# Kernel tuning notes

Hardware: AMD Instinct MI355X
Metric: run time of the kernel (lower is better)

## Reference

```python
import jax, jax.numpy as jnp
import numpy as np

H = 50  # hidden_size
IN = 3  # input_size
OUT = 7


def _lstm_layer(x, Wih, Whh, bih, bhh):
    # x: [B, T, D]; Wih: [4H, D]; Whh: [4H, H]; biases: [4H]
    # Precompute input-side gate pre-activations once (torch adds both biases).
    xg = jnp.einsum('btd,gd->btg', x, Wih) + bih + bhh  # [B, T, 4H]
    B = x.shape[0]
    h0 = jnp.zeros((B, H), x.dtype)
    c0 = jnp.zeros((B, H), x.dtype)

    def step(carry, xt):
        h, c = carry
        gates = xt + h @ Whh.T  # [B, 4H]
        i, f, g, o = jnp.split(gates, 4, axis=-1)  # torch gate order: i,f,g,o
        i = jax.nn.sigmoid(i)
        f = jax.nn.sigmoid(f)
        g = jnp.tanh(g)
        o = jax.nn.sigmoid(o)
        c = f * c + i * g
        h = o * jnp.tanh(c)
        return (h, c), h

    (_, _), hs = jax.lax.scan(step, (h0, c0), jnp.swapaxes(xg, 0, 1))  # hs: [T, B, H]
    return jnp.swapaxes(hs, 0, 1)  # [B, T, H]


def setup_inputs() -> dict:
    key = jax.random.key(0)
    ks = jax.random.split(key, 11)
    s = 1.0 / np.sqrt(H)  # torch LSTM init scale
    B, T = 4096, 512
    return {
        'x': jax.random.normal(ks[0], (B, T, IN), jnp.float32),
        'Wih0': jax.random.uniform(ks[1], (4 * H, IN), jnp.float32, -s, s),
        'Whh0': jax.random.uniform(ks[2], (4 * H, H), jnp.float32, -s, s),
        'bih0': jax.random.uniform(ks[3], (4 * H,), jnp.float32, -s, s),
        'bhh0': jax.random.uniform(ks[4], (4 * H,), jnp.float32, -s, s),
        'Wih1': jax.random.uniform(ks[5], (4 * H, H), jnp.float32, -s, s),
        'Whh1': jax.random.uniform(ks[6], (4 * H, H), jnp.float32, -s, s),
        'bih1': jax.random.uniform(ks[7], (4 * H,), jnp.float32, -s, s),
        'bhh1': jax.random.uniform(ks[8], (4 * H,), jnp.float32, -s, s),
        'Wfc': jax.random.uniform(ks[9], (OUT, H), jnp.float32, -s, s),
        'bfc': jax.random.uniform(ks[10], (OUT,), jnp.float32, -s, s),
    }


def reference(x, Wih0, Whh0, bih0, bhh0, Wih1, Whh1, bih1, bhh1, Wfc, bfc):
    h1 = _lstm_layer(x, Wih0, Whh0, bih0, bhh0)   # [B, T, H]
    h2 = _lstm_layer(h1, Wih1, Whh1, bih1, bhh1)  # [B, T, H]
    last = h2[:, -1, :]                           # [B, H]
    return last @ Wfc.T + bfc                     # [B, 7]
```

## Files before the change

kernel.cpp:

```cpp
#include <hip/hip_runtime.h>

#define HD 50
#define TT 512
#define BRR 16
#define TC 32
#define HS 72

using f16   = _Float16;
using f16x8 = __attribute__((ext_vector_type(8))) f16;
using f32x4 = __attribute__((ext_vector_type(4))) float;

__device__ __forceinline__ short f2h_bits(float f) {
    f16 h = (f16)f;
    return *reinterpret_cast<short*>(&h);
}
__device__ __forceinline__ float h2f(short b) {
    f16 h = *reinterpret_cast<f16*>(&b);
    return (float)h;
}
__device__ __forceinline__ float frcp(float x) { return __builtin_amdgcn_rcpf(x); }
__device__ __forceinline__ float sigf(float x) { return frcp(1.0f + __expf(-x)); }
__device__ __forceinline__ float tanhfast(float x) {
    return 1.0f - 2.0f * frcp(__expf(2.0f * x) + 1.0f);
}

__global__ __launch_bounds__(512, 2) void lstm2_f16(
    const float* __restrict__ x,
    const float* __restrict__ Wih0, const float* __restrict__ Whh0,
    const float* __restrict__ bih0, const float* __restrict__ bhh0,
    const float* __restrict__ Wih1, const float* __restrict__ Whh1,
    const float* __restrict__ bih1, const float* __restrict__ bhh1,
    const float* __restrict__ Wfc, const float* __restrict__ bfc,
    float* __restrict__ out)
{
    __shared__ short s_h0[2][BRR][HS];
    __shared__ short s_h1[2][BRR][HS];
    __shared__ float s_xs[2][BRR][TC*3];

    const int tid  = threadIdx.x;
    const int wid  = tid >> 6;
    const int lane = tid & 63;
    const int lr   = lane & 15;
    const int lq   = lane >> 4;
    const int r0   = blockIdx.x * BRR;
    const bool pathA = (wid < 4);
    const int  wsub  = wid & 3;
    const int  u     = lr * 4 + wsub;
    const bool valid = (u < HD);

    f16x8 bw[4][4];
    float bvT[4];
    #pragma unroll
    for (int tt = 0; tt < 4; ++tt) {
        #pragma unroll
        for (int s = 0; s < 4; ++s) bw[tt][s] = (f16x8)0;
        const int g = tt * HD + (valid ? u : 0);
        if (pathA) {
            bvT[tt] = valid ? bih0[g] + bhh0[g] : 0.f;
            #pragma unroll
            for (int s = 0; s < 2; ++s) {
                #pragma unroll
                for (int j = 0; j < 8; ++j) {
                    const int k = s*32 + lq*8 + j;
                    float wv = 0.f;
                    if (valid) {
                        if (k < HD) wv = Whh0[g*HD + k];
                        else if (k < HD+3) wv = Wih0[g*3 + (k-HD)];
                    }
                    bw[tt][s][j] = (f16)wv;
                }
            }
        } else {
            bvT[tt] = valid ? bih1[g] + bhh1[g] : 0.f;
            #pragma unroll
            for (int s = 0; s < 4; ++s) {
                #pragma unroll
                for (int j = 0; j < 8; ++j) {
                    const int k = s*32 + lq*8 + j;
                    float wv = 0.f;
                    if (valid) {
                        if (k < HD) wv = Wih1[g*HD + k];
                        else if (k >= 64 && k < 64+HD) wv = Whh1[g*HD + (k-64)];
                    }
                    bw[tt][s][j] = (f16)wv;
                }
            }
        }
    }

    float cst[4] = {0.f, 0.f, 0.f, 0.f};

    const bool xth = (tid < 48);
    const int  xr  = tid / 3, xd = tid % 3;

    for (int p = tid; p < 2*BRR*HS; p += 512) {
        ((short*)s_h0)[p] = 0; ((short*)s_h1)[p] = 0;
    }
    for (int p = tid; p < BRR*TC*3; p += 512) {
        const int rr = p / (TC*3), q = p % (TC*3);
        s_xs[0][rr][q] = x[(size_t)(r0+rr)*(TT*3) + q];
    }
    __syncthreads();
    if (xth) {
        s_h0[1][xr][HD+xd] = f2h_bits(s_xs[0][xr][xd]);
    }
    __syncthreads();

    for (int n = 0; n <= TT; ++n) {
        if (pathA) {
            if (n < TT) {
                const char* hb0 = (const char*)&s_h0[(n+1)&1][0][0];
                f16x8 ah[2];
                #pragma unroll
                for (int s = 0; s < 2; ++s) {
                    const int off = lr*(2*HS) + s*64 + lq*16;
                    ah[s] = *(const f16x8*)(hb0 + off);
                }
                f32x4 acc[4];
                #pragma unroll
                for (int tt = 0; tt < 4; ++tt) { const float b = bvT[tt]; acc[tt] = (f32x4){b,b,b,b}; }
                #pragma unroll
                for (int s = 0; s < 2; ++s) {
                    #pragma unroll
                    for (int tt = 0; tt < 4; ++tt)
                        acc[tt] = __builtin_amdgcn_mfma_f32_16x16x32_f16(ah[s], bw[tt][s], acc[tt], 0,0,0);
                }
                if (valid) {
                    #pragma unroll
                    for (int j = 0; j < 4; ++j) {
                        const float iv = sigf(acc[0][j]);
                        const float fv = sigf(acc[1][j]);
                        const float gv = tanhfast(acc[2][j]);
                        const float ov = sigf(acc[3][j]);
                        const float c  = fv*cst[j] + iv*gv;
                        cst[j] = c;
                        const float h  = ov*tanhfast(c);
                        s_h0[n&1][lq*4+j][u] = f2h_bits(h);
                    }
                }
            }
            if (xth && (n+1) < TT) {
                const int tn = n + 1;
                s_h0[n&1][xr][HD+xd] = f2h_bits(s_xs[(tn/TC)&1][xr][(tn%TC)*3 + xd]);
            }
        } else {
            if (n >= 1) {
                const char* hb0 = (const char*)&s_h0[(n+1)&1][0][0];
                const char* hb1 = (const char*)&s_h1[n&1][0][0];
                f16x8 ah[4];
                #pragma unroll
                for (int s = 0; s < 2; ++s) {
                    const int off = lr*(2*HS) + s*64 + lq*16;
                    ah[s]   = *(const f16x8*)(hb0 + off);
                    ah[2+s] = *(const f16x8*)(hb1 + off);
                }
                f32x4 acc[4];
                #pragma unroll
                for (int tt = 0; tt < 4; ++tt) { const float b = bvT[tt]; acc[tt] = (f32x4){b,b,b,b}; }
                #pragma unroll
                for (int s = 0; s < 4; ++s) {
                    #pragma unroll
                    for (int tt = 0; tt < 4; ++tt)
                        acc[tt] = __builtin_amdgcn_mfma_f32_16x16x32_f16(ah[s], bw[tt][s], acc[tt], 0,0,0);
                }
                if (valid) {
                    #pragma unroll
                    for (int j = 0; j < 4; ++j) {
                        const float iv = sigf(acc[0][j]);
                        const float fv = sigf(acc[1][j]);
                        const float gv = tanhfast(acc[2][j]);
                        const float ov = sigf(acc[3][j]);
                        const float c  = fv*cst[j] + iv*gv;
                        cst[j] = c;
                        const float h  = ov*tanhfast(c);
                        s_h1[(n+1)&1][lq*4+j][u] = f2h_bits(h);
                    }
                }
            }
        }
        {
            const int t2s = n + 2;
            if (t2s < TT && (t2s % TC) == 0) {
                const int cb = (t2s / TC) & 1;
                for (int p = tid; p < BRR*TC*3; p += 512) {
                    const int rr = p / (TC*3), q = p % (TC*3);
                    s_xs[cb][rr][q] = x[(size_t)(r0+rr)*(TT*3) + (size_t)t2s*3 + q];
                }
            }
        }
        __syncthreads();
    }

    if (tid < BRR*7) {
        const int r = tid / 7, o = tid % 7;
        float acc = bfc[o];
        #pragma unroll
        for (int uu = 0; uu < HD; ++uu)
            acc += h2f(s_h1[1][r][uu]) * Wfc[o*HD + uu];
        out[(size_t)(r0+r)*7 + o] = acc;
    }
}

extern "C" void kernel_launch(void* const* d_in, const int* in_sizes, int n_in,
                              void* d_out, int out_size, void* d_ws, size_t ws_size,
                              hipStream_t stream) {
    const float* xp    = (const float*)d_in[0];
    const float* Wih0  = (const float*)d_in[1];
    const float* Whh0  = (const float*)d_in[2];
    const float* bih0  = (const float*)d_in[3];
    const float* bhh0  = (const float*)d_in[4];
    const float* Wih1  = (const float*)d_in[5];
    const float* Whh1  = (const float*)d_in[6];
    const float* bih1  = (const float*)d_in[7];
    const float* bhh1  = (const float*)d_in[8];
    const float* Wfc   = (const float*)d_in[9];
    const float* bfc   = (const float*)d_in[10];
    float* outp = (float*)d_out;

    const int B = in_sizes[0] / (TT * 3);
    const int grid = B / BRR;

    lstm2_f16<<<grid, 512, 0, stream>>>(
        xp, Wih0, Whh0, bih0, bhh0, Wih1, Whh1, bih1, bhh1, Wfc, bfc, outp);
}
```

Before: 443.7 us.

## Unify both LSTM layers into one shared-memory operand and uniform wave work

Merges the layer-0 and layer-1 hidden states into a single shared buffer so every wave runs the same 16 MFMAs over a combined K=128 operand. Gate units of both layers are interleaved across all eight waves instead of splitting waves by layer, which balances the work per step. The log2(e) scaling is folded into the weights and biases so the activations use exp2 directly. The x chunk staging buffer is dropped in favour of a per-step global load by a few lanes. The trade is that layer-0 waves now issue redundant MFMAs over zero-padded columns, and the per-step global load of x sits on the serial critical path.

```diff
diff --git a/kernel.cpp b/kernel.cpp
--- a/kernel.cpp
+++ b/kernel.cpp
@@ -3,12 +3,13 @@
 #define HD 50
 #define TT 512
 #define BRR 16
-#define TC 32
-#define HS 72
+#define KS 136
 
 using f16   = _Float16;
 using f16x8 = __attribute__((ext_vector_type(8))) f16;
 using f32x4 = __attribute__((ext_vector_type(4))) float;
+
+#define LOG2E 1.4426950408889634f
 
 __device__ __forceinline__ short f2h_bits(float f) {
     f16 h = (f16)f;
@@ -19,12 +20,13 @@
     return (float)h;
 }
 __device__ __forceinline__ float frcp(float x) { return __builtin_amdgcn_rcpf(x); }
-__device__ __forceinline__ float sigf(float x) { return frcp(1.0f + __expf(-x)); }
-__device__ __forceinline__ float tanhfast(float x) {
-    return 1.0f - 2.0f * frcp(__expf(2.0f * x) + 1.0f);
-}
+#if __has_builtin(__builtin_amdgcn_exp2f)
+__device__ __forceinline__ float fexp2(float x) { return __builtin_amdgcn_exp2f(x); }
+#else
+__device__ __forceinline__ float fexp2(float x) { return exp2f(x); }
+#endif
 
-__global__ __launch_bounds__(512, 2) void lstm2_f16(
+__global__ __launch_bounds__(512, 2) void lstm2_uni(
     const float* __restrict__ x,
     const float* __restrict__ Wih0, const float* __restrict__ Whh0,
     const float* __restrict__ bih0, const float* __restrict__ bhh0,
@@ -33,9 +35,7 @@
     const float* __restrict__ Wfc, const float* __restrict__ bfc,
     float* __restrict__ out)
 {
-    __shared__ short s_h0[2][BRR][HS];
-    __shared__ short s_h1[2][BRR][HS];
-    __shared__ float s_xs[2][BRR][TC*3];
+    __shared__ short sA[2][BRR][KS];
 
     const int tid  = threadIdx.x;
     const int wid  = tid >> 6;
@@ -43,35 +43,21 @@
     const int lr   = lane & 15;
     const int lq   = lane >> 4;
     const int r0   = blockIdx.x * BRR;
-    const bool pathA = (wid < 4);
-    const int  wsub  = wid & 3;
-    const int  u     = lr * 4 + wsub;
-    const bool valid = (u < HD);
+
+    const int  p     = 8 * lr + wid;
+    const bool valid = (p < 100);
+    const bool isL1  = valid && (p >= 50);
+    const int  u     = valid ? (isL1 ? p - 50 : p) : 0;
+    const int  wcol  = isL1 ? 64 + u : u;
 
     f16x8 bw[4][4];
     float bvT[4];
     #pragma unroll
     for (int tt = 0; tt < 4; ++tt) {
-        #pragma unroll
-        for (int s = 0; s < 4; ++s) bw[tt][s] = (f16x8)0;
-        const int g = tt * HD + (valid ? u : 0);
-        if (pathA) {
-            bvT[tt] = valid ? bih0[g] + bhh0[g] : 0.f;
-            #pragma unroll
-            for (int s = 0; s < 2; ++s) {
-                #pragma unroll
-                for (int j = 0; j < 8; ++j) {
-                    const int k = s*32 + lq*8 + j;
-                    float wv = 0.f;
-                    if (valid) {
-                        if (k < HD) wv = Whh0[g*HD + k];
-                        else if (k < HD+3) wv = Wih0[g*3 + (k-HD)];
-                    }
-                    bw[tt][s][j] = (f16)wv;
-                }
-            }
-        } else {
-            bvT[tt] = valid ? bih1[g] + bhh1[g] : 0.f;
+        const float sc = (tt == 2) ? (2.0f * LOG2E) : (-LOG2E);
+        const int g = tt * HD + u;
+        if (!isL1) {
+            bvT[tt] = valid ? (bih0[g] + bhh0[g]) * sc : 0.f;
             #pragma unroll
             for (int s = 0; s < 4; ++s) {
                 #pragma unroll
@@ -79,10 +65,23 @@
                     const int k = s*32 + lq*8 + j;
                     float wv = 0.f;
                     if (valid) {
-                        if (k < HD) wv = Wih1[g*HD + k];
-                        else if (k >= 64 && k < 64+HD) wv = Whh1[g*HD + (k-64)];
+                        if (k < HD) wv = Whh0[g*HD + k];
+                        else if (k < HD + 3) wv = Wih0[g*3 + (k - HD)];
                     }
-                    bw[tt][s][j] = (f16)wv;
+                    bw[tt][s][j] = (f16)(wv * sc);
+                }
+            }
+        } else {
+            bvT[tt] = (bih1[g] + bhh1[g]) * sc;
+            #pragma unroll
+            for (int s = 0; s < 4; ++s) {
+                #pragma unroll
+                for (int j = 0; j < 8; ++j) {
+                    const int k = s*32 + lq*8 + j;
+                    float wv = 0.f;
+                    if (k < HD) wv = Wih1[g*HD + k];
+                    else if (k >= 64 && k < 64 + HD) wv = Whh1[g*HD + (k - 64)];
+                    bw[tt][s][j] = (f16)(wv * sc);
                 }
             }
         }
@@ -90,114 +89,61 @@
 
     float cst[4] = {0.f, 0.f, 0.f, 0.f};
 
-    const bool xth = (tid < 48);
-    const int  xr  = tid / 3, xd = tid % 3;
+    const bool xduty = (wid < 4) && (lr >= 13);
+    const int  xidx  = wid * 12 + (lr - 13) * 4 + lq;
+    const int  xrow  = xidx / 3, xd = xidx % 3;
 
-    for (int p = tid; p < 2*BRR*HS; p += 512) {
-        ((short*)s_h0)[p] = 0; ((short*)s_h1)[p] = 0;
-    }
-    for (int p = tid; p < BRR*TC*3; p += 512) {
-        const int rr = p / (TC*3), q = p % (TC*3);
-        s_xs[0][rr][q] = x[(size_t)(r0+rr)*(TT*3) + q];
-    }
+    for (int q = tid; q < 2 * BRR * KS; q += 512) ((short*)sA)[q] = 0;
     __syncthreads();
-    if (xth) {
-        s_h0[1][xr][HD+xd] = f2h_bits(s_xs[0][xr][xd]);
-    }
+    if (xduty) sA[0][xrow][HD + xd] = f2h_bits(x[(size_t)(r0 + xrow) * (TT*3) + xd]);
     __syncthreads();
 
     for (int n = 0; n <= TT; ++n) {
-        if (pathA) {
-            if (n < TT) {
-                const char* hb0 = (const char*)&s_h0[(n+1)&1][0][0];
-                f16x8 ah[2];
-                #pragma unroll
-                for (int s = 0; s < 2; ++s) {
-                    const int off = lr*(2*HS) + s*64 + lq*16;
-                    ah[s] = *(const f16x8*)(hb0 + off);
-                }
-                f32x4 acc[4];
-                #pragma unroll
-                for (int tt = 0; tt < 4; ++tt) { const float b = bvT[tt]; acc[tt] = (f32x4){b,b,b,b}; }
-                #pragma unroll
-                for (int s = 0; s < 2; ++s) {
-                    #pragma unroll
-                    for (int tt = 0; tt < 4; ++tt)
-                        acc[tt] = __builtin_amdgcn_mfma_f32_16x16x32_f16(ah[s], bw[tt][s], acc[tt], 0,0,0);
-                }
-                if (valid) {
-                    #pragma unroll
-                    for (int j = 0; j < 4; ++j) {
-                        const float iv = sigf(acc[0][j]);
-                        const float fv = sigf(acc[1][j]);
-                        const float gv = tanhfast(acc[2][j]);
-                        const float ov = sigf(acc[3][j]);
-                        const float c  = fv*cst[j] + iv*gv;
-                        cst[j] = c;
-                        const float h  = ov*tanhfast(c);
-                        s_h0[n&1][lq*4+j][u] = f2h_bits(h);
-                    }
-                }
-            }
-            if (xth && (n+1) < TT) {
-                const int tn = n + 1;
-                s_h0[n&1][xr][HD+xd] = f2h_bits(s_xs[(tn/TC)&1][xr][(tn%TC)*3 + xd]);
-            }
-        } else {
-            if (n >= 1) {
-                const char* hb0 = (const char*)&s_h0[(n+1)&1][0][0];
-                const char* hb1 = (const char*)&s_h1[n&1][0][0];
-                f16x8 ah[4];
-                #pragma unroll
-                for (int s = 0; s < 2; ++s) {
-                    const int off = lr*(2*HS) + s*64 + lq*16;
-                    ah[s]   = *(const f16x8*)(hb0 + off);
-                    ah[2+s] = *(const f16x8*)(hb1 + off);
-                }
-                f32x4 acc[4];
-                #pragma unroll
-                for (int tt = 0; tt < 4; ++tt) { const float b = bvT[tt]; acc[tt] = (f32x4){b,b,b,b}; }
-                #pragma unroll
-                for (int s = 0; s < 4; ++s) {
-                    #pragma unroll
-                    for (int tt = 0; tt < 4; ++tt)
-                        acc[tt] = __builtin_amdgcn_mfma_f32_16x16x32_f16(ah[s], bw[tt][s], acc[tt], 0,0,0);
-                }
-                if (valid) {
-                    #pragma unroll
-                    for (int j = 0; j < 4; ++j) {
-                        const float iv = sigf(acc[0][j]);
-                        const float fv = sigf(acc[1][j]);
-                        const float gv = tanhfast(acc[2][j]);
-                        const float ov = sigf(acc[3][j]);
-                        const float c  = fv*cst[j] + iv*gv;
-                        cst[j] = c;
-                        const float h  = ov*tanhfast(c);
-                        s_h1[(n+1)&1][lq*4+j][u] = f2h_bits(h);
-                    }
-                }
+        float xv = 0.f;
+        const bool xact = xduty && (n + 1) < TT;
+        if (xact) xv = x[(size_t)(r0 + xrow) * (TT*3) + (size_t)(n + 1) * 3 + xd];
+
+        const char* ab = (const char*)&sA[n & 1][0][0];
+        f16x8 a[4];
+        #pragma unroll
+        for (int s = 0; s < 4; ++s)
+            a[s] = *(const f16x8*)(ab + lr * (2 * KS) + s * 64 + lq * 16);
+        f32x4 acc[4];
+        #pragma unroll
+        for (int tt = 0; tt < 4; ++tt) { const float b = bvT[tt]; acc[tt] = (f32x4){b, b, b, b}; }
+        #pragma unroll
+        for (int s = 0; s < 4; ++s) {
+            #pragma unroll
+            for (int tt = 0; tt < 4; ++tt)
+                acc[tt] = __builtin_amdgcn_mfma_f32_16x16x32_f16(a[s], bw[tt][s], acc[tt], 0, 0, 0);
+        }
+
+        const bool act = valid && (isL1 ? (n >= 1) : (n < TT));
+        if (act) {
+            #pragma unroll
+            for (int j = 0; j < 4; ++j) {
+                const float iv = frcp(1.0f + fexp2(acc[0][j]));
+                const float fv = frcp(1.0f + fexp2(acc[1][j]));
+                const float gv = 1.0f - 2.0f * frcp(1.0f + fexp2(acc[2][j]));
+                const float ov = frcp(1.0f + fexp2(acc[3][j]));
+                const float c  = fv * cst[j] + iv * gv;
+                cst[j] = c;
+                const float th = 1.0f - 2.0f * frcp(1.0f + fexp2(c * (2.0f * LOG2E)));
+                const float h  = ov * th;
+                sA[(n + 1) & 1][lq * 4 + j][wcol] = f2h_bits(h);
             }
         }
-        {
-            const int t2s = n + 2;
-            if (t2s < TT && (t2s % TC) == 0) {
-                const int cb = (t2s / TC) & 1;
-                for (int p = tid; p < BRR*TC*3; p += 512) {
-                    const int rr = p / (TC*3), q = p % (TC*3);
-                    s_xs[cb][rr][q] = x[(size_t)(r0+rr)*(TT*3) + (size_t)t2s*3 + q];
-                }
-            }
-        }
+        if (xact) sA[(n + 1) & 1][xrow][HD + xd] = f2h_bits(xv);
         __syncthreads();
     }
 
-    if (tid < BRR*7) {
+    if (tid < BRR * 7) {
         const int r = tid / 7, o = tid % 7;
         float acc = bfc[o];
         #pragma unroll
         for (int uu = 0; uu < HD; ++uu)
-            acc += h2f(s_h1[1][r][uu]) * Wfc[o*HD + uu];
-        out[(size_t)(r0+r)*7 + o] = acc;
+            acc += h2f(sA[1][r][64 + uu]) * Wfc[o * HD + uu];
+        out[(size_t)(r0 + r) * 7 + o] = acc;
     }
 }
 
@@ -220,6 +166,6 @@
     const int B = in_sizes[0] / (TT * 3);
     const int grid = B / BRR;
 
-    lstm2_f16<<<grid, 512, 0, stream>>>(
+    lstm2_uni<<<grid, 512, 0, stream>>>(
         xp, Wih0, Whh0, bih0, bhh0, Wih1, Whh1, bih1, bhh1, Wfc, bfc, outp);
 }
```

Result: faster. 420.6 us (-5.2%).
